# Performance work log

Measured on AMD Instinct MI355X. Metric: run time of the kernel, lower is better.

## Reference

```python
import jax, jax.numpy as jnp
import numpy as np

B = 64  # number of graph pairs in the batch


def gcn_conv(x, W, b, edge_index, n_nodes):
    """PyG GCNConv: add self-loops, symmetric deg^-1/2 normalization, x@W then aggregate."""
    h = x @ W  # [N, out]
    src = jnp.concatenate([edge_index[0], jnp.arange(n_nodes)])
    dst = jnp.concatenate([edge_index[1], jnp.arange(n_nodes)])
    deg = jax.ops.segment_sum(jnp.ones_like(dst, dtype=h.dtype), dst, num_segments=n_nodes)
    dinv = jnp.where(deg > 0, jax.lax.rsqrt(jnp.maximum(deg, 1e-12)), 0.0)
    coef = dinv[src] * dinv[dst]  # [E+N]
    out = jax.ops.segment_sum(coef[:, None] * h[src], dst, num_segments=n_nodes)
    return out + b


def mean_pool(x, batch, num_graphs):
    sums = jax.ops.segment_sum(x, batch, num_segments=num_graphs)
    cnts = jax.ops.segment_sum(jnp.ones((x.shape[0],), x.dtype), batch, num_segments=num_graphs)
    return sums / jnp.maximum(cnts, 1.0)[:, None]


def setup_inputs() -> dict:
    key = jax.random.key(0)
    ks = jax.random.split(key, 32)
    n_prot, e_prot, n_mol, e_mol = 100000, 1600000, 4096, 16384

    def lin(k, fin, fout):
        k1, k2 = jax.random.split(k)
        s = 1.0 / np.sqrt(fin)
        return (jax.random.uniform(k1, (fin, fout), jnp.float32, -s, s),
                jax.random.uniform(k2, (fout,), jnp.float32, -s, s))

    fc1_w, fc1_b = lin(ks[0], 18640, 128)
    fc2_w, fc2_b = lin(ks[1], 128, 128)
    fcm1_w, fcm1_b = lin(ks[2], 21, 64)
    fcm2_w, fcm2_b = lin(ks[3], 64, 64)
    gp1_w, gp1_b = lin(ks[4], 9, 128)
    gp2_w, gp2_b = lin(ks[5], 128, 128)
    gm1_w, gm1_b = lin(ks[6], 9, 128)
    gm2_w, gm2_b = lin(ks[7], 128, 128)
    fcc_w, fcc_b = lin(ks[8], 448, 128)
    out_w, out_b = lin(ks[9], 128, 2)

    return {
        "metadata_prot": jax.random.normal(ks[10], (B, 18640), jnp.float32),
        "metadata_mol": jax.random.normal(ks[11], (B, 21), jnp.float32),
        "x_prot": jax.random.normal(ks[12], (n_prot, 9), jnp.float32),
        "x_mol": jax.random.normal(ks[13], (n_mol, 9), jnp.float32),
        "edge_index_prot": jax.random.randint(ks[14], (2, e_prot), 0, n_prot),
        "batch_vector_prot": jnp.sort(jax.random.randint(ks[15], (n_prot,), 0, B)),
        "edge_index_mol": jax.random.randint(ks[16], (2, e_mol), 0, n_mol),
        "batch_vector_mol": jnp.sort(jax.random.randint(ks[17], (n_mol,), 0, B)),
        "fc1_w": fc1_w, "fc1_b": fc1_b, "fc2_w": fc2_w, "fc2_b": fc2_b,
        "fcm1_w": fcm1_w, "fcm1_b": fcm1_b, "fcm2_w": fcm2_w, "fcm2_b": fcm2_b,
        "gp1_w": gp1_w, "gp1_b": gp1_b, "gp2_w": gp2_w, "gp2_b": gp2_b,
        "gm1_w": gm1_w, "gm1_b": gm1_b, "gm2_w": gm2_w, "gm2_b": gm2_b,
        "fcc_w": fcc_w, "fcc_b": fcc_b, "out_w": out_w, "out_b": out_b,
    }


def reference(metadata_prot, metadata_mol, x_prot, x_mol,
              edge_index_prot, batch_vector_prot, edge_index_mol, batch_vector_mol,
              fc1_w, fc1_b, fc2_w, fc2_b, fcm1_w, fcm1_b, fcm2_w, fcm2_b,
              gp1_w, gp1_b, gp2_w, gp2_b, gm1_w, gm1_b, gm2_w, gm2_b,
              fcc_w, fcc_b, out_w, out_b):
    relu = jax.nn.relu
    mp = relu(relu(metadata_prot @ fc1_w + fc1_b) @ fc2_w + fc2_b)
    mm = relu(relu(metadata_mol @ fcm1_w + fcm1_b) @ fcm2_w + fcm2_b)

    n_prot = x_prot.shape[0]
    hp = relu(gcn_conv(x_prot, gp1_w, gp1_b, edge_index_prot, n_prot))
    hp = relu(gcn_conv(hp, gp2_w, gp2_b, edge_index_prot, n_prot))
    hp = mean_pool(hp, batch_vector_prot, B)

    n_mol = x_mol.shape[0]
    hm = relu(gcn_conv(x_mol, gm1_w, gm1_b, edge_index_mol, n_mol))
    hm = relu(gcn_conv(hm, gm2_w, gm2_b, edge_index_mol, n_mol))
    hm = mean_pool(hm, batch_vector_mol, B)

    combined = jnp.concatenate([mp, mm, hp, hm], axis=1)  # [B, 448]
    combined = relu(combined @ fcc_w + fcc_b)
    return relu(combined @ out_w + out_b)  # [B, 2]
```

## Files before the change

kernel.cpp:

```cpp
#include <hip/hip_runtime.h>

#define CAP 64
#define GB  64
#define FC1K 18640
#define CH 932
#define KS 20
#define NRP 8

typedef __attribute__((ext_vector_type(8))) short bf16x8;
typedef __attribute__((ext_vector_type(4))) float f32x4;

static inline int cdiv(long a, long b){ return (int)((a + b - 1) / b); }

__device__ inline unsigned short pack_bf1(float a) {
  unsigned ua = __float_as_uint(a); ua += 0x7fffu + ((ua >> 16) & 1u);
  return (unsigned short)(ua >> 16);
}
__device__ inline unsigned pack_bf2(float a, float b) {
  unsigned ua = __float_as_uint(a); ua += 0x7fffu + ((ua >> 16) & 1u);
  unsigned ub = __float_as_uint(b); ub += 0x7fffu + ((ub >> 16) & 1u);
  return (ua >> 16) | (ub & 0xffff0000u);
}
__device__ inline float unpack_lo(unsigned short u) { return __uint_as_float(((unsigned)u) << 16); }

__global__ void k_mega(
                       const float* __restrict__ md, const float* __restrict__ fc1w,
                       float* __restrict__ part,
                       const int* __restrict__ ei_m, int EM,
                       int* __restrict__ cnt_m, int* __restrict__ idx_m, int MOLB,
                       const int* __restrict__ bv_p, int NP,
                       const int* __restrict__ bv_m, int NM,
                       float* __restrict__ cntp, float* __restrict__ cntm,
                       const int* __restrict__ ei_p, int EP, int step,
                       int* __restrict__ cnt_p, int* __restrict__ idx_p) {
  __shared__ float smd[64][KS];
  int bid = blockIdx.x;
  int tid = threadIdx.x;

  if (bid < CH) {
    int c = bid;
    int k0 = c * KS;
    for (int t = tid; t < 64 * KS; t += 256) {
      int b = t / KS, k = t % KS;
      smd[b][k] = md[(size_t)b * FC1K + k0 + k];
    }
    __syncthreads();
    int j = tid & 127, bg = tid >> 7;
    float acc[32];
    #pragma unroll
    for (int i = 0; i < 32; i++) acc[i] = 0.f;
    for (int k = 0; k < KS; k++) {
      float w = fc1w[(size_t)(k0 + k) * 128 + j];
      #pragma unroll
      for (int i = 0; i < 32; i++) acc[i] += smd[bg * 32 + i][k] * w;
    }
    float* dst = part + ((size_t)c * 64 + bg * 32) * 128 + j;
    #pragma unroll
    for (int i = 0; i < 32; i++) dst[(size_t)i * 128] = acc[i];
    return;
  }
  bid -= CH;

  if (bid < MOLB) {
    int e = bid * 256 + tid;
    if (e < EM) {
      int s = ei_m[e], d = ei_m[EM + e];
      int c = atomicAdd(&cnt_m[d], 1);
      if (c < CAP) idx_m[d * CAP + c] = s;
    }
    return;
  }
  bid -= MOLB;

  if (bid == 0) {
    if (tid < 128) {
      const int* batch; float* cnt; int n, b;
      if (tid < 64) { batch = bv_p; n = NP; cnt = cntp; b = tid; }
      else          { batch = bv_m; n = NM; cnt = cntm; b = tid - 64; }
      int lo = 0, hi = n;
      while (lo < hi) { int mid = (lo + hi) >> 1; if (batch[mid] < b) lo = mid + 1; else hi = mid; }
      int start = lo;
      lo = 0; hi = n;
      while (lo < hi) { int mid = (lo + hi) >> 1; if (batch[mid] <= b) lo = mid + 1; else hi = mid; }
      cnt[b] = (float)(lo - start);
    }
    return;
  }
  bid -= 1;

  {
    int r = bid & 7;
    int lo = r * step, hi = lo + step; if (hi > NP) hi = NP;
    long eb = (long)(bid >> 3) * 1024 + tid;
    int d0 = -1, d1 = -1, d2 = -1, d3 = -1;
    if (eb       < EP) d0 = ei_p[EP + eb];
    if (eb + 256 < EP) d1 = ei_p[EP + eb + 256];
    if (eb + 512 < EP) d2 = ei_p[EP + eb + 512];
    if (eb + 768 < EP) d3 = ei_p[EP + eb + 768];
    bool a0 = (d0 >= lo) & (d0 < hi);
    bool a1 = (d1 >= lo) & (d1 < hi);
    bool a2 = (d2 >= lo) & (d2 < hi);
    bool a3 = (d3 >= lo) & (d3 < hi);
    int s0 = a0 ? ei_p[eb]       : 0;
    int s1 = a1 ? ei_p[eb + 256] : 0;
    int s2 = a2 ? ei_p[eb + 512] : 0;
    int s3 = a3 ? ei_p[eb + 768] : 0;
    if (a0) { int c = atomicAdd(&cnt_p[d0], 1); if (c < CAP) idx_p[d0 * CAP + c] = s0; }
    if (a1) { int c = atomicAdd(&cnt_p[d1], 1); if (c < CAP) idx_p[d1 * CAP + c] = s1; }
    if (a2) { int c = atomicAdd(&cnt_p[d2], 1); if (c < CAP) idx_p[d2 * CAP + c] = s2; }
    if (a3) { int c = atomicAdd(&cnt_p[d3], 1); if (c < CAP) idx_p[d3 * CAP + c] = s3; }
  }
}

__global__ void k_dinv_xs2(const int* __restrict__ cnt_p, const float* __restrict__ x_p,
                           float* __restrict__ dinv_p, unsigned short* __restrict__ xs_p, int np,
                           const int* __restrict__ cnt_m, const float* __restrict__ x_m,
                           float* __restrict__ dinv_m, unsigned short* __restrict__ xs_m, int nm) {
  int t = blockIdx.x * blockDim.x + threadIdx.x;
  const int* cnt; const float* x; float* dinv; unsigned short* xs; int v, f;
  int tp = np * 16;
  if (t < tp) { v = t >> 4; f = t & 15; cnt = cnt_p; x = x_p; dinv = dinv_p; xs = xs_p; }
  else {
    t -= tp;
    if (t >= nm * 16) return;
    v = t >> 4; f = t & 15; cnt = cnt_m; x = x_m; dinv = dinv_m; xs = xs_m;
  }
  float d = rsqrtf((float)cnt[v] + 1.0f);
  if (f == 0) dinv[v] = d;
  xs[(size_t)v * 16 + f] = (f < 9) ? pack_bf1(d * x[(size_t)v * 9 + f]) : (unsigned short)0;
}

__global__ void k_gather9x2(const unsigned short* __restrict__ xs_p, const float* __restrict__ dinv_p,
                            const int* __restrict__ cnt_p, const int* __restrict__ idx_p,
                            float* __restrict__ ax_p, int np,
                            const unsigned short* __restrict__ xs_m, const float* __restrict__ dinv_m,
                            const int* __restrict__ cnt_m, const int* __restrict__ idx_m,
                            float* __restrict__ ax_m, int nm, int PB) {
  const unsigned short* xs; const float* dinv; const int* cnt; const int* idx; float* ax; int n; long t;
  if ((int)blockIdx.x < PB) {
    xs = xs_p; dinv = dinv_p; cnt = cnt_p; idx = idx_p; ax = ax_p; n = np;
    t = (long)blockIdx.x * 256 + threadIdx.x;
  } else {
    xs = xs_m; dinv = dinv_m; cnt = cnt_m; idx = idx_m; ax = ax_m; n = nm;
    t = (long)(blockIdx.x - PB) * 256 + threadIdx.x;
  }
  int v = (int)(t >> 4), f = (int)(t & 15);
  if (v >= n) return;
  int deg = cnt[v]; if (deg > CAP) deg = CAP;
  const int* idxv = idx + (size_t)v * CAP;
  float acc = unpack_lo(xs[(size_t)v * 16 + f]);
  int p = 0;
  for (; p + 4 <= deg; p += 4) {
    int s0 = idxv[p], s1 = idxv[p + 1], s2 = idxv[p + 2], s3 = idxv[p + 3];
    float a0 = unpack_lo(xs[(size_t)s0 * 16 + f]);
    float a1 = unpack_lo(xs[(size_t)s1 * 16 + f]);
    float a2 = unpack_lo(xs[(size_t)s2 * 16 + f]);
    float a3 = unpack_lo(xs[(size_t)s3 * 16 + f]);
    acc += a0; acc += a1; acc += a2; acc += a3;
  }
  for (; p < deg; p++) acc += unpack_lo(xs[(size_t)idxv[p] * 16 + f]);
  ax[(size_t)v * 16 + f] = dinv[v] * acc;
}

__global__ void k_fused_lin2(const float* __restrict__ ax_p, const float* __restrict__ W1p,
                             const float* __restrict__ b1p, const float* __restrict__ W2p,
                             const float* __restrict__ dinv_p, unsigned* __restrict__ hout_p, int np,
                             const float* __restrict__ ax_m, const float* __restrict__ W1m,
                             const float* __restrict__ b1m, const float* __restrict__ W2m,
                             const float* __restrict__ dinv_m, unsigned* __restrict__ hout_m, int nm,
                             int PB) {
  __shared__ float W1s[9 * 128];
  __shared__ float b1s[128];
  __shared__ float axs[16][16];
  __shared__ uint4 As4[256];
  const float* ax; const float* W1; const float* b1; const float* W2; const float* dinv;
  unsigned* hout; int n, tile0, gsz;
  if ((int)blockIdx.x < PB) {
    ax = ax_p; W1 = W1p; b1 = b1p; W2 = W2p; dinv = dinv_p; hout = hout_p; n = np;
    tile0 = blockIdx.x; gsz = PB;
  } else {
    ax = ax_m; W1 = W1m; b1 = b1m; W2 = W2m; dinv = dinv_m; hout = hout_m; n = nm;
    tile0 = blockIdx.x - PB; gsz = gridDim.x - PB;
  }
  int ntiles = (n + 15) >> 4;
  int tid = threadIdx.x;
  int lane = tid & 63;
  int wave = tid >> 6;
  int l15 = lane & 15;
  int lg  = lane >> 4;

  for (int i = tid; i < 9 * 128; i += 256) W1s[i] = W1[i];
  if (tid < 128) b1s[tid] = b1[tid];

  bf16x8 bfrag[2][4];
  #pragma unroll
  for (int ct = 0; ct < 2; ct++) {
    int col = wave * 32 + ct * 16 + l15;
    #pragma unroll
    for (int ks = 0; ks < 4; ks++) {
      #pragma unroll
      for (int j = 0; j < 8; j++) {
        int k = ks * 32 + lg * 8 + j;
        bfrag[ct][ks][j] = (short)pack_bf1(W2[(size_t)k * 128 + col]);
      }
    }
  }
  __syncthreads();

  int r = tid >> 4, c4 = tid & 15;
  for (int tile = tile0; tile < ntiles; tile += gsz) {
    int base = tile * 16;
    int v = base + r;
    axs[r][c4] = (v < n) ? ax[(size_t)v * 16 + c4] : 0.f;
    __syncthreads();

    float h[8];
    int j0 = c4 * 8;
    #pragma unroll
    for (int jj = 0; jj < 8; jj++) h[jj] = b1s[j0 + jj];
    #pragma unroll
    for (int k = 0; k < 9; k++) {
      float a = axs[r][k];
      #pragma unroll
      for (int jj = 0; jj < 8; jj++) h[jj] += a * W1s[k * 128 + j0 + jj];
    }
    uint4 av;
    av.x = pack_bf2(fmaxf(h[0], 0.f), fmaxf(h[1], 0.f));
    av.y = pack_bf2(fmaxf(h[2], 0.f), fmaxf(h[3], 0.f));
    av.z = pack_bf2(fmaxf(h[4], 0.f), fmaxf(h[5], 0.f));
    av.w = pack_bf2(fmaxf(h[6], 0.f), fmaxf(h[7], 0.f));
    As4[r * 16 + (c4 ^ r)] = av;
    __syncthreads();

    bf16x8 afr[4];
    #pragma unroll
    for (int ks = 0; ks < 4; ks++) {
      uint4 a4 = As4[l15 * 16 + (((ks * 4) + lg) ^ l15)];
      afr[ks] = *(bf16x8*)&a4;
    }

    f32x4 acc0 = {0.f, 0.f, 0.f, 0.f}, acc1 = {0.f, 0.f, 0.f, 0.f};
    #pragma unroll
    for (int ks = 0; ks < 4; ks++) {
      acc0 = __builtin_amdgcn_mfma_f32_16x16x32_bf16(afr[ks], bfrag[0][ks], acc0, 0, 0, 0);
      acc1 = __builtin_amdgcn_mfma_f32_16x16x32_bf16(afr[ks], bfrag[1][ks], acc1, 0, 0, 0);
    }

    #pragma unroll
    for (int reg = 0; reg < 4; reg++) {
      int row = lg * 4 + reg;
      int ov = base + row;
      if (ov < n) {
        float dv = dinv[ov];
        unsigned short* hp16 = (unsigned short*)hout;
        hp16[(size_t)ov * 128 + wave * 32 + l15]      = pack_bf1(dv * acc0[reg]);
        hp16[(size_t)ov * 128 + wave * 32 + 16 + l15] = pack_bf1(dv * acc1[reg]);
      }
    }
    __syncthreads();
  }
}

__global__ void k_gather_bf2(const unsigned* __restrict__ hb_p, const float* __restrict__ dinv_p,
                             const int* __restrict__ cnt_p, const int* __restrict__ idx_p,
                             const float* __restrict__ bias_p, unsigned* __restrict__ out_p, int np,
                             const unsigned* __restrict__ hb_m, const float* __restrict__ dinv_m,
                             const int* __restrict__ cnt_m, const int* __restrict__ idx_m,
                             const float* __restrict__ bias_m, unsigned* __restrict__ out_m, int nm,
                             int PB) {
  const unsigned* hb; const float* dinv; const int* cnt; const int* idx;
  const float* bias; unsigned* out; int n; long t;
  if ((int)blockIdx.x < PB) {
    hb = hb_p; dinv = dinv_p; cnt = cnt_p; idx = idx_p; bias = bias_p; out = out_p; n = np;
    t = (long)blockIdx.x * 256 + threadIdx.x;
  } else {
    hb = hb_m; dinv = dinv_m; cnt = cnt_m; idx = idx_m; bias = bias_m; out = out_m; n = nm;
    t = (long)(blockIdx.x - PB) * 256 + threadIdx.x;
  }
  int v = (int)(t >> 6), f = (int)(t & 63);
  if (v >= n) return;
  float dv = dinv[v];
  int deg = cnt[v]; if (deg > CAP) deg = CAP;
  const int* idxv = idx + (size_t)v * CAP;
  unsigned u = hb[(size_t)v * 64 + f];
  float accL = __uint_as_float(u << 16);
  float accH = __uint_as_float(u & 0xffff0000u);
  int p = 0;
  for (; p + 8 <= deg; p += 8) {
    int s0 = idxv[p], s1 = idxv[p+1], s2 = idxv[p+2], s3 = idxv[p+3];
    int s4 = idxv[p+4], s5 = idxv[p+5], s6 = idxv[p+6], s7 = idxv[p+7];
    unsigned u0 = hb[(size_t)s0 * 64 + f];
    unsigned u1 = hb[(size_t)s1 * 64 + f];
    unsigned u2 = hb[(size_t)s2 * 64 + f];
    unsigned u3 = hb[(size_t)s3 * 64 + f];
    unsigned u4 = hb[(size_t)s4 * 64 + f];
    unsigned u5 = hb[(size_t)s5 * 64 + f];
    unsigned u6 = hb[(size_t)s6 * 64 + f];
    unsigned u7 = hb[(size_t)s7 * 64 + f];
    accL += __uint_as_float(u0 << 16); accH += __uint_as_float(u0 & 0xffff0000u);
    accL += __uint_as_float(u1 << 16); accH += __uint_as_float(u1 & 0xffff0000u);
    accL += __uint_as_float(u2 << 16); accH += __uint_as_float(u2 & 0xffff0000u);
    accL += __uint_as_float(u3 << 16); accH += __uint_as_float(u3 & 0xffff0000u);
    accL += __uint_as_float(u4 << 16); accH += __uint_as_float(u4 & 0xffff0000u);
    accL += __uint_as_float(u5 << 16); accH += __uint_as_float(u5 & 0xffff0000u);
    accL += __uint_as_float(u6 << 16); accH += __uint_as_float(u6 & 0xffff0000u);
    accL += __uint_as_float(u7 << 16); accH += __uint_as_float(u7 & 0xffff0000u);
  }
  for (; p < deg; p++) {
    int s = idxv[p];
    unsigned uu = hb[(size_t)s * 64 + f];
    accL += __uint_as_float(uu << 16); accH += __uint_as_float(uu & 0xffff0000u);
  }
  float2 b2 = *(const float2*)&bias[2 * f];
  float ox = fmaxf(dv * accL + b2.x, 0.f);
  float oy = fmaxf(dv * accH + b2.y, 0.f);
  out[(size_t)v * 64 + f] = pack_bf2(ox, oy);
}

__global__ void k_pool_bf2(const unsigned* __restrict__ h_p, const int* __restrict__ batch_p,
                           float* __restrict__ sums_p, int np,
                           const unsigned* __restrict__ h_m, const int* __restrict__ batch_m,
                           float* __restrict__ sums_m, int nm, int PB) {
  const unsigned* h; const int* batch; float* sums; int n; long v0;
  if ((int)blockIdx.x < PB) {
    h = h_p; batch = batch_p; sums = sums_p; n = np; v0 = (long)blockIdx.x * 64;
  } else {
    h = h_m; batch = batch_m; sums = sums_m; n = nm; v0 = (long)(blockIdx.x - PB) * 64;
  }
  int f = threadIdx.x;
  if (v0 >= n) return;
  long v1 = v0 + 64; if (v1 > n) v1 = n;
  int cur = batch[v0];
  float acc = 0.f;
  for (long v = v0; v < v1; ++v) {
    int bv = batch[v];
    if (bv != cur) { atomicAdd(&sums[cur * 128 + f], acc); acc = 0.f; cur = bv; }
    unsigned u = h[(size_t)v * 64 + (f >> 1)];
    acc += (f & 1) ? __uint_as_float(u & 0xffff0000u) : __uint_as_float(u << 16);
  }
  atomicAdd(&sums[cur * 128 + f], acc);
}

__global__ void k_mlp2_fc(const float* __restrict__ part, const float* __restrict__ b1,
                          const float* __restrict__ W2, const float* __restrict__ b2,
                          float* __restrict__ out) {
  __shared__ float red[8][128];
  __shared__ float row[128];
  int b = blockIdx.x, tid = threadIdx.x;
  int j = tid & 127, kg = tid >> 7;
  float acc = 0.f;
  #pragma unroll 4
  for (int c = kg; c < CH; c += 8) acc += part[((size_t)c * 64 + b) * 128 + j];
  red[kg][j] = acc;
  __syncthreads();
  if (kg == 0) {
    float s = red[0][j] + red[1][j] + red[2][j] + red[3][j]
            + red[4][j] + red[5][j] + red[6][j] + red[7][j];
    row[j] = fmaxf(s + b1[j], 0.f);
  }
  __syncthreads();
  float a2 = 0.f;
  int k0 = kg * 16;
  #pragma unroll
  for (int k = k0; k < k0 + 16; k++) a2 += row[k] * W2[k * 128 + j];
  red[kg][j] = a2;
  __syncthreads();
  if (kg == 0) {
    float s = red[0][j] + red[1][j] + red[2][j] + red[3][j]
            + red[4][j] + red[5][j] + red[6][j] + red[7][j];
    out[b * 128 + j] = fmaxf(s + b2[j], 0.f);
  }
}

__global__ void k_fcc_final(const float* __restrict__ mp,
                            const float* __restrict__ md_mol,
                            const float* __restrict__ fcm1_w, const float* __restrict__ fcm1_b,
                            const float* __restrict__ fcm2_w, const float* __restrict__ fcm2_b,
                            const float* __restrict__ hpS, const float* __restrict__ hmS,
                            const float* __restrict__ cntp, const float* __restrict__ cntm,
                            const float* __restrict__ W, const float* __restrict__ bias,
                            const float* __restrict__ outw, const float* __restrict__ outb,
                            float* __restrict__ out) {
  __shared__ float row[448];
  __shared__ float mrow[21];
  __shared__ float h1m[64];
  __shared__ float red[8][128];
  __shared__ float frow[128];
  int b = blockIdx.x, tid = threadIdx.x;
  int j = tid & 127, kg = tid >> 7;
  if (tid < 21) mrow[tid] = md_mol[b * 21 + tid];
  if (tid < 128) row[tid] = mp[b * 128 + tid];
  else if (tid >= 192 && tid < 320) row[tid] = hpS[b * 128 + (tid - 192)] / fmaxf(cntp[b], 1.f);
  else if (tid >= 320 && tid < 448) row[tid] = hmS[b * 128 + (tid - 320)] / fmaxf(cntm[b], 1.f);
  __syncthreads();
  if (tid < 64) {
    float a = fcm1_b[tid];
    #pragma unroll 7
    for (int k = 0; k < 21; k++) a += mrow[k] * fcm1_w[k * 64 + tid];
    h1m[tid] = fmaxf(a, 0.f);
  }
  __syncthreads();
  if (tid < 64) {
    float a = fcm2_b[tid];
    #pragma unroll 8
    for (int k = 0; k < 64; k++) a += h1m[k] * fcm2_w[k * 64 + tid];
    row[128 + tid] = fmaxf(a, 0.f);
  }
  __syncthreads();
  float acc = 0.f;
  int k0 = kg * 56;
  #pragma unroll 8
  for (int k = k0; k < k0 + 56; k++) acc += row[k] * W[k * 128 + j];
  red[kg][j] = acc;
  __syncthreads();
  if (kg == 0) {
    float s = red[0][j] + red[1][j] + red[2][j] + red[3][j]
            + red[4][j] + red[5][j] + red[6][j] + red[7][j];
    frow[j] = fmaxf(s + bias[j], 0.f);
  }
  __syncthreads();
  if (tid < 128) {
    int o = tid >> 6, l = tid & 63;
    float p = frow[l] * outw[l * 2 + o] + frow[64 + l] * outw[(64 + l) * 2 + o];
    #pragma unroll
    for (int off = 32; off; off >>= 1) p += __shfl_down(p, off);
    if (l == 0) out[b * 2 + o] = fmaxf(p + outb[o], 0.f);
  }
}

extern "C" void kernel_launch(void* const* d_in, const int* in_sizes, int n_in,
                              void* d_out, int out_size, void* d_ws, size_t ws_size,
                              hipStream_t stream) {
  const float* md_prot = (const float*)d_in[0];
  const float* md_mol  = (const float*)d_in[1];
  const float* x_prot  = (const float*)d_in[2];
  const float* x_mol   = (const float*)d_in[3];
  const int*   ei_p    = (const int*)d_in[4];
  const int*   bv_p    = (const int*)d_in[5];
  const int*   ei_m    = (const int*)d_in[6];
  const int*   bv_m    = (const int*)d_in[7];
  const float* fc1_w = (const float*)d_in[8],  * fc1_b = (const float*)d_in[9];
  const float* fc2_w = (const float*)d_in[10], * fc2_b = (const float*)d_in[11];
  const float* fcm1_w= (const float*)d_in[12], * fcm1_b= (const float*)d_in[13];
  const float* fcm2_w= (const float*)d_in[14], * fcm2_b= (const float*)d_in[15];
  const float* gp1_w = (const float*)d_in[16], * gp1_b = (const float*)d_in[17];
  const float* gp2_w = (const float*)d_in[18], * gp2_b = (const float*)d_in[19];
  const float* gm1_w = (const float*)d_in[20], * gm1_b = (const float*)d_in[21];
  const float* gm2_w = (const float*)d_in[22], * gm2_b = (const float*)d_in[23];
  const float* fcc_w = (const float*)d_in[24], * fcc_b = (const float*)d_in[25];
  const float* out_w = (const float*)d_in[26], * out_b = (const float*)d_in[27];

  const int NP = in_sizes[2] / 9;
  const int EP = in_sizes[4] / 2;
  const int NM = in_sizes[3] / 9;
  const int EM = in_sizes[6] / 2;
  const int MOLB = cdiv(EM, 256);

  char* w = (char*)d_ws;
  size_t off = 0;
  auto take = [&](size_t bytes) -> void* {
    void* p = w + off;
    off = (off + bytes + 255) & ~(size_t)255;
    return p;
  };
  char*     big    = (char*)take((size_t)NP * 128 * 4);
  float*    part   = (float*)big;
  unsigned* hbf_p  = (unsigned*)big;
  unsigned* obf_p  = (unsigned*)(big + (size_t)NP * 64 * 4);
  unsigned short* xs_p = (unsigned short*)take((size_t)NP * 16 * 2);
  float*    ax_p   = (float*)take((size_t)NP * 16 * 4);
  int*      idx_p  = (int*)  take((size_t)NP * CAP * 4);
  float*    dinv_p = (float*)take((size_t)NP * 4);
  unsigned short* xs_m = (unsigned short*)take((size_t)NM * 16 * 2);
  float*    ax_m   = (float*)take((size_t)NM * 16 * 4);
  unsigned* hbf_m  = (unsigned*)take((size_t)NM * 64 * 4);
  unsigned* obf_m  = (unsigned*)take((size_t)NM * 64 * 4);
  int*      idx_m  = (int*)  take((size_t)NM * CAP * 4);
  float*    dinv_m = (float*)take((size_t)NM * 4);
  float*    mp     = (float*)take(GB * 128 * 4);
  size_t zb_cnt_p = (size_t)NP * 4;
  size_t zb_cnt_m = (size_t)NM * 4;
  size_t zb_hp    = (size_t)GB * 128 * 4;
  size_t zb_hm    = (size_t)GB * 128 * 4;
  size_t zb_cp    = (size_t)GB * 4;
  size_t zb_cm    = (size_t)GB * 4;
  char* zr = (char*)take(zb_cnt_p + zb_cnt_m + zb_hp + zb_hm + zb_cp + zb_cm);
  int*   cnt_p = (int*)zr;
  int*   cnt_m = (int*)(zr + zb_cnt_p);
  float* hp    = (float*)(zr + zb_cnt_p + zb_cnt_m);
  float* hm    = (float*)(zr + zb_cnt_p + zb_cnt_m + zb_hp);
  float* cntp  = (float*)(zr + zb_cnt_p + zb_cnt_m + zb_hp + zb_hm);
  float* cntm  = (float*)(zr + zb_cnt_p + zb_cnt_m + zb_hp + zb_hm + zb_cp);
  (void)ws_size; (void)n_in; (void)out_size;

  hipMemsetAsync(zr, 0, zb_cnt_p + zb_cnt_m + zb_hp + zb_hm + zb_cp + zb_cm, stream);

  {
    int step = cdiv(NP, NRP);
    int PFB  = 8 * cdiv(EP, 1024);
    k_mega<<<CH + MOLB + 1 + PFB, 256, 0, stream>>>(
        md_prot, fc1_w, part,
        ei_m, EM, cnt_m, idx_m, MOLB,
        bv_p, NP, bv_m, NM, cntp, cntm,
        ei_p, EP, step, cnt_p, idx_p);
  }

  k_mlp2_fc<<<GB, 1024, 0, stream>>>(part, fc1_b, fc2_w, fc2_b, mp);

  k_dinv_xs2<<<cdiv((long)(NP + NM) * 16, 256), 256, 0, stream>>>(
      cnt_p, x_prot, dinv_p, xs_p, NP, cnt_m, x_mol, dinv_m, xs_m, NM);

  {
    int PB9 = cdiv((long)NP * 16, 256);
    k_gather9x2<<<PB9 + cdiv((long)NM * 16, 256), 256, 0, stream>>>(
        xs_p, dinv_p, cnt_p, idx_p, ax_p, NP, xs_m, dinv_m, cnt_m, idx_m, ax_m, NM, PB9);
  }
  k_fused_lin2<<<1024 + 256, 256, 0, stream>>>(
      ax_p, gp1_w, gp1_b, gp2_w, dinv_p, hbf_p, NP,
      ax_m, gm1_w, gm1_b, gm2_w, dinv_m, hbf_m, NM, 1024);
  {
    int PBg = cdiv((long)NP * 64, 256);
    k_gather_bf2<<<PBg + cdiv((long)NM * 64, 256), 256, 0, stream>>>(
        hbf_p, dinv_p, cnt_p, idx_p, gp2_b, obf_p, NP,
        hbf_m, dinv_m, cnt_m, idx_m, gm2_b, obf_m, NM, PBg);
  }
  {
    int PBp = cdiv(NP, 64);
    k_pool_bf2<<<PBp + cdiv(NM, 64), 128, 0, stream>>>(
        obf_p, bv_p, hp, NP, obf_m, bv_m, hm, NM, PBp);
  }

  k_fcc_final<<<GB, 1024, 0, stream>>>(mp, md_mol, fcm1_w, fcm1_b, fcm2_w, fcm2_b,
                                       hp, hm, cntp, cntm,
                                       fcc_w, fcc_b, out_w, out_b, (float*)d_out);
}
```

Before: 263.4 us.

## Fuse first-layer gather into GCN linear kernel and merge MLP with dinv prep

The 9-feature neighbour gather is moved into the fused linear kernel, so the per-tile aggregate goes straight to shared memory and the ax intermediate buffer plus its launch disappear. The metadata MLP reduction is merged into the dinv/xs preparation kernel as extra blocks, removing another launch. The GCN1 grid doubles its protein blocks to cover the added gather latency. In exchange, the gather now runs inside a tile loop followed by a barrier, which may serialise latency differently than the standalone gather did.

Result: no change. 265.4 us, median of 2 (+0.7%).

```diff
diff --git a/kernel.cpp b/kernel.cpp
--- a/kernel.cpp
+++ b/kernel.cpp
@@ -23,8 +23,7 @@
 }
 __device__ inline float unpack_lo(unsigned short u) { return __uint_as_float(((unsigned)u) << 16); }
 
-__global__ void k_mega(
-                       const float* __restrict__ md, const float* __restrict__ fc1w,
+__global__ void k_mega(const float* __restrict__ md, const float* __restrict__ fc1w,
                        float* __restrict__ part,
                        const int* __restrict__ ei_m, int EM,
                        int* __restrict__ cnt_m, int* __restrict__ idx_m, int MOLB,
@@ -112,74 +111,79 @@
   }
 }
 
-__global__ void k_dinv_xs2(const int* __restrict__ cnt_p, const float* __restrict__ x_p,
-                           float* __restrict__ dinv_p, unsigned short* __restrict__ xs_p, int np,
-                           const int* __restrict__ cnt_m, const float* __restrict__ x_m,
-                           float* __restrict__ dinv_m, unsigned short* __restrict__ xs_m, int nm) {
-  int t = blockIdx.x * blockDim.x + threadIdx.x;
+__global__ void k_prep(const float* __restrict__ part, const float* __restrict__ b1,
+                       const float* __restrict__ W2, const float* __restrict__ b2,
+                       float* __restrict__ mp,
+                       const int* __restrict__ cnt_p, const float* __restrict__ x_p,
+                       float* __restrict__ dinv_p, unsigned short* __restrict__ xs_p, int np,
+                       const int* __restrict__ cnt_m, const float* __restrict__ x_m,
+                       float* __restrict__ dinv_m, unsigned short* __restrict__ xs_m, int nm) {
+  __shared__ float red[8][128];
+  __shared__ float row[128];
+  int bid = blockIdx.x, tid = threadIdx.x;
+  if (bid < GB) {
+    int b = bid;
+    int j = tid & 127, kg = tid >> 7;
+    float acc = 0.f;
+    #pragma unroll 4
+    for (int c = kg; c < CH; c += 8) acc += part[((size_t)c * 64 + b) * 128 + j];
+    red[kg][j] = acc;
+    __syncthreads();
+    if (kg == 0) {
+      float s = red[0][j] + red[1][j] + red[2][j] + red[3][j]
+              + red[4][j] + red[5][j] + red[6][j] + red[7][j];
+      row[j] = fmaxf(s + b1[j], 0.f);
+    }
+    __syncthreads();
+    float a2 = 0.f;
+    int k0 = kg * 16;
+    #pragma unroll
+    for (int k = k0; k < k0 + 16; k++) a2 += row[k] * W2[k * 128 + j];
+    red[kg][j] = a2;
+    __syncthreads();
+    if (kg == 0) {
+      float s = red[0][j] + red[1][j] + red[2][j] + red[3][j]
+              + red[4][j] + red[5][j] + red[6][j] + red[7][j];
+      mp[b * 128 + j] = fmaxf(s + b2[j], 0.f);
+    }
+    return;
+  }
+  long t = (long)(bid - GB) * 1024 + tid;
   const int* cnt; const float* x; float* dinv; unsigned short* xs; int v, f;
-  int tp = np * 16;
-  if (t < tp) { v = t >> 4; f = t & 15; cnt = cnt_p; x = x_p; dinv = dinv_p; xs = xs_p; }
+  long tp = (long)np * 16;
+  if (t < tp) { v = (int)(t >> 4); f = (int)(t & 15); cnt = cnt_p; x = x_p; dinv = dinv_p; xs = xs_p; }
   else {
     t -= tp;
-    if (t >= nm * 16) return;
-    v = t >> 4; f = t & 15; cnt = cnt_m; x = x_m; dinv = dinv_m; xs = xs_m;
+    if (t >= (long)nm * 16) return;
+    v = (int)(t >> 4); f = (int)(t & 15); cnt = cnt_m; x = x_m; dinv = dinv_m; xs = xs_m;
   }
   float d = rsqrtf((float)cnt[v] + 1.0f);
   if (f == 0) dinv[v] = d;
   xs[(size_t)v * 16 + f] = (f < 9) ? pack_bf1(d * x[(size_t)v * 9 + f]) : (unsigned short)0;
 }
 
-__global__ void k_gather9x2(const unsigned short* __restrict__ xs_p, const float* __restrict__ dinv_p,
-                            const int* __restrict__ cnt_p, const int* __restrict__ idx_p,
-                            float* __restrict__ ax_p, int np,
-                            const unsigned short* __restrict__ xs_m, const float* __restrict__ dinv_m,
-                            const int* __restrict__ cnt_m, const int* __restrict__ idx_m,
-                            float* __restrict__ ax_m, int nm, int PB) {
-  const unsigned short* xs; const float* dinv; const int* cnt; const int* idx; float* ax; int n; long t;
-  if ((int)blockIdx.x < PB) {
-    xs = xs_p; dinv = dinv_p; cnt = cnt_p; idx = idx_p; ax = ax_p; n = np;
-    t = (long)blockIdx.x * 256 + threadIdx.x;
-  } else {
-    xs = xs_m; dinv = dinv_m; cnt = cnt_m; idx = idx_m; ax = ax_m; n = nm;
-    t = (long)(blockIdx.x - PB) * 256 + threadIdx.x;
-  }
-  int v = (int)(t >> 4), f = (int)(t & 15);
-  if (v >= n) return;
-  int deg = cnt[v]; if (deg > CAP) deg = CAP;
-  const int* idxv = idx + (size_t)v * CAP;
-  float acc = unpack_lo(xs[(size_t)v * 16 + f]);
-  int p = 0;
-  for (; p + 4 <= deg; p += 4) {
-    int s0 = idxv[p], s1 = idxv[p + 1], s2 = idxv[p + 2], s3 = idxv[p + 3];
-    float a0 = unpack_lo(xs[(size_t)s0 * 16 + f]);
-    float a1 = unpack_lo(xs[(size_t)s1 * 16 + f]);
-    float a2 = unpack_lo(xs[(size_t)s2 * 16 + f]);
-    float a3 = unpack_lo(xs[(size_t)s3 * 16 + f]);
-    acc += a0; acc += a1; acc += a2; acc += a3;
-  }
-  for (; p < deg; p++) acc += unpack_lo(xs[(size_t)idxv[p] * 16 + f]);
-  ax[(size_t)v * 16 + f] = dinv[v] * acc;
-}
-
-__global__ void k_fused_lin2(const float* __restrict__ ax_p, const float* __restrict__ W1p,
-                             const float* __restrict__ b1p, const float* __restrict__ W2p,
-                             const float* __restrict__ dinv_p, unsigned* __restrict__ hout_p, int np,
-                             const float* __restrict__ ax_m, const float* __restrict__ W1m,
-                             const float* __restrict__ b1m, const float* __restrict__ W2m,
-                             const float* __restrict__ dinv_m, unsigned* __restrict__ hout_m, int nm,
-                             int PB) {
+__global__ void k_gcn1(const unsigned short* __restrict__ xs_p, const float* __restrict__ dinv_p,
+                       const int* __restrict__ cnt_p, const int* __restrict__ idx_p,
+                       const float* __restrict__ W1p, const float* __restrict__ b1p,
+                       const float* __restrict__ W2p, unsigned* __restrict__ hout_p, int np,
+                       const unsigned short* __restrict__ xs_m, const float* __restrict__ dinv_m,
+                       const int* __restrict__ cnt_m, const int* __restrict__ idx_m,
+                       const float* __restrict__ W1m, const float* __restrict__ b1m,
+                       const float* __restrict__ W2m, unsigned* __restrict__ hout_m, int nm,
+                       int PB) {
   __shared__ float W1s[9 * 128];
   __shared__ float b1s[128];
   __shared__ float axs[16][16];
   __shared__ uint4 As4[256];
-  const float* ax; const float* W1; const float* b1; const float* W2; const float* dinv;
-  unsigned* hout; int n, tile0, gsz;
+  const unsigned short* xs; const float* dinv; const int* cnt; const int* idx;
+  const float* W1; const float* b1; const float* W2; unsigned* hout; int n, tile0, gsz;
   if ((int)blockIdx.x < PB) {
-    ax = ax_p; W1 = W1p; b1 = b1p; W2 = W2p; dinv = dinv_p; hout = hout_p; n = np;
+    xs = xs_p; dinv = dinv_p; cnt = cnt_p; idx = idx_p;
+    W1 = W1p; b1 = b1p; W2 = W2p; hout = hout_p; n = np;
     tile0 = blockIdx.x; gsz = PB;
   } else {
-    ax = ax_m; W1 = W1m; b1 = b1m; W2 = W2m; dinv = dinv_m; hout = hout_m; n = nm;
+    xs = xs_m; dinv = dinv_m; cnt = cnt_m; idx = idx_m;
+    W1 = W1m; b1 = b1m; W2 = W2m; hout = hout_m; n = nm;
     tile0 = blockIdx.x - PB; gsz = gridDim.x - PB;
   }
   int ntiles = (n + 15) >> 4;
@@ -211,7 +215,24 @@
   for (int tile = tile0; tile < ntiles; tile += gsz) {
     int base = tile * 16;
     int v = base + r;
-    axs[r][c4] = (v < n) ? ax[(size_t)v * 16 + c4] : 0.f;
+    float acc = 0.f;
+    if (v < n) {
+      int deg = cnt[v]; if (deg > CAP) deg = CAP;
+      const int* idxv = idx + (size_t)v * CAP;
+      acc = unpack_lo(xs[(size_t)v * 16 + c4]);
+      int p = 0;
+      for (; p + 4 <= deg; p += 4) {
+        int s0 = idxv[p], s1 = idxv[p + 1], s2 = idxv[p + 2], s3 = idxv[p + 3];
+        float a0 = unpack_lo(xs[(size_t)s0 * 16 + c4]);
+        float a1 = unpack_lo(xs[(size_t)s1 * 16 + c4]);
+        float a2 = unpack_lo(xs[(size_t)s2 * 16 + c4]);
+        float a3 = unpack_lo(xs[(size_t)s3 * 16 + c4]);
+        acc += a0; acc += a1; acc += a2; acc += a3;
+      }
+      for (; p < deg; p++) acc += unpack_lo(xs[(size_t)idxv[p] * 16 + c4]);
+      acc *= dinv[v];
+    }
+    axs[r][c4] = acc;
     __syncthreads();
 
     float h[8];
@@ -341,37 +362,6 @@
   atomicAdd(&sums[cur * 128 + f], acc);
 }
 
-__global__ void k_mlp2_fc(const float* __restrict__ part, const float* __restrict__ b1,
-                          const float* __restrict__ W2, const float* __restrict__ b2,
-                          float* __restrict__ out) {
-  __shared__ float red[8][128];
-  __shared__ float row[128];
-  int b = blockIdx.x, tid = threadIdx.x;
-  int j = tid & 127, kg = tid >> 7;
-  float acc = 0.f;
-  #pragma unroll 4
-  for (int c = kg; c < CH; c += 8) acc += part[((size_t)c * 64 + b) * 128 + j];
-  red[kg][j] = acc;
-  __syncthreads();
-  if (kg == 0) {
-    float s = red[0][j] + red[1][j] + red[2][j] + red[3][j]
-            + red[4][j] + red[5][j] + red[6][j] + red[7][j];
-    row[j] = fmaxf(s + b1[j], 0.f);
-  }
-  __syncthreads();
-  float a2 = 0.f;
-  int k0 = kg * 16;
-  #pragma unroll
-  for (int k = k0; k < k0 + 16; k++) a2 += row[k] * W2[k * 128 + j];
-  red[kg][j] = a2;
-  __syncthreads();
-  if (kg == 0) {
-    float s = red[0][j] + red[1][j] + red[2][j] + red[3][j]
-            + red[4][j] + red[5][j] + red[6][j] + red[7][j];
-    out[b * 128 + j] = fmaxf(s + b2[j], 0.f);
-  }
-}
-
 __global__ void k_fcc_final(const float* __restrict__ mp,
                             const float* __restrict__ md_mol,
                             const float* __restrict__ fcm1_w, const float* __restrict__ fcm1_b,
@@ -468,11 +458,9 @@
   unsigned* hbf_p  = (unsigned*)big;
   unsigned* obf_p  = (unsigned*)(big + (size_t)NP * 64 * 4);
   unsigned short* xs_p = (unsigned short*)take((size_t)NP * 16 * 2);
-  float*    ax_p   = (float*)take((size_t)NP * 16 * 4);
   int*      idx_p  = (int*)  take((size_t)NP * CAP * 4);
   float*    dinv_p = (float*)take((size_t)NP * 4);
   unsigned short* xs_m = (unsigned short*)take((size_t)NM * 16 * 2);
-  float*    ax_m   = (float*)take((size_t)NM * 16 * 4);
   unsigned* hbf_m  = (unsigned*)take((size_t)NM * 64 * 4);
   unsigned* obf_m  = (unsigned*)take((size_t)NM * 64 * 4);
   int*      idx_m  = (int*)  take((size_t)NM * CAP * 4);
@@ -505,19 +493,15 @@
         ei_p, EP, step, cnt_p, idx_p);
   }
 
-  k_mlp2_fc<<<GB, 1024, 0, stream>>>(part, fc1_b, fc2_w, fc2_b, mp);
-
-  k_dinv_xs2<<<cdiv((long)(NP + NM) * 16, 256), 256, 0, stream>>>(
-      cnt_p, x_prot, dinv_p, xs_p, NP, cnt_m, x_mol, dinv_m, xs_m, NM);
-
-  {
-    int PB9 = cdiv((long)NP * 16, 256);
-    k_gather9x2<<<PB9 + cdiv((long)NM * 16, 256), 256, 0, stream>>>(
-        xs_p, dinv_p, cnt_p, idx_p, ax_p, NP, xs_m, dinv_m, cnt_m, idx_m, ax_m, NM, PB9);
-  }
-  k_fused_lin2<<<1024 + 256, 256, 0, stream>>>(
-      ax_p, gp1_w, gp1_b, gp2_w, dinv_p, hbf_p, NP,
-      ax_m, gm1_w, gm1_b, gm2_w, dinv_m, hbf_m, NM, 1024);
+  k_prep<<<GB + cdiv((long)(NP + NM) * 16, 1024), 1024, 0, stream>>>(
+      part, fc1_b, fc2_w, fc2_b, mp,
+      cnt_p, x_prot, dinv_p, xs_p, NP,
+      cnt_m, x_mol, dinv_m, xs_m, NM);
+
+  k_gcn1<<<2048 + 256, 256, 0, stream>>>(
+      xs_p, dinv_p, cnt_p, idx_p, gp1_w, gp1_b, gp2_w, hbf_p, NP,
+      xs_m, dinv_m, cnt_m, idx_m, gm1_w, gm1_b, gm2_w, hbf_m, NM, 2048);
+
   {
     int PBg = cdiv((long)NP * 64, 256);
     k_gather_bf2<<<PBg + cdiv((long)NM * 64, 256), 256, 0, stream>>>(
```
